# Kernel optimization log

Measured on AMD Instinct MI355X. Metric: run time of the kernel, lower is better.

Reference implementation:

```python
import jax, jax.numpy as jnp
import numpy as np

B, S, D = 4, 2048, 1024
H, DK = 16, 64
NUM_BUCKETS = 32
MAX_DISTANCE = 128
EPS = 1e-6


def _relative_position_bucket(q_len, kv_len):
    # causal (bidirectional=False) T5 bucketization
    ctx = jnp.arange(q_len, dtype=jnp.int32)[:, None]
    mem = jnp.arange(kv_len, dtype=jnp.int32)[None, :]
    rp = mem - ctx                       # [q, kv]
    rp = -jnp.minimum(rp, 0)             # nonnegative distances to the past
    max_exact = NUM_BUCKETS // 2
    is_small = rp < max_exact
    rp_safe = jnp.maximum(rp, 1).astype(jnp.float32)
    large = max_exact + (
        jnp.log(rp_safe / max_exact) / np.log(MAX_DISTANCE / max_exact) * (NUM_BUCKETS - max_exact)
    ).astype(jnp.int32)
    large = jnp.minimum(large, NUM_BUCKETS - 1)
    return jnp.where(is_small, rp, large)  # [q, kv] int32 in [0, NUM_BUCKETS)


def setup_inputs() -> dict:
    key = jax.random.key(0)
    k1, k2, k3, k4 = jax.random.split(key, 4)
    hidden_states = jax.random.normal(k1, (B, S, D), dtype=jnp.float32)
    sequence_mask = jnp.ones((B, S), dtype=bool)
    rms_w = jnp.ones((D,), dtype=jnp.float32)
    W_qkv = jax.random.normal(k2, (D, 3 * H * DK), dtype=jnp.float32) * (D ** -0.5)
    W_o = jax.random.normal(k3, (H * DK, D), dtype=jnp.float32) * ((H * DK) ** -0.5)
    rel_bias = jax.random.normal(k4, (NUM_BUCKETS, H), dtype=jnp.float32)
    return {"hidden_states": hidden_states, "sequence_mask": sequence_mask,
            "rms_w": rms_w, "W_qkv": W_qkv, "W_o": W_o, "rel_bias": rel_bias}


def reference(hidden_states, sequence_mask, rms_w, W_qkv, W_o, rel_bias):
    # RMSNorm
    var = jnp.mean(hidden_states * hidden_states, axis=-1, keepdims=True)
    normed = hidden_states * jax.lax.rsqrt(var + EPS) * rms_w

    # QKV projection -> [B, S, 3, H, DK] -> [B, H, S, DK] each
    qkv = (normed @ W_qkv).reshape(B, S, 3, H, DK)
    q = jnp.transpose(qkv[:, :, 0], (0, 2, 1, 3))
    k = jnp.transpose(qkv[:, :, 1], (0, 2, 1, 3))
    v = jnp.transpose(qkv[:, :, 2], (0, 2, 1, 3))

    # relative position bias: gather [S,S,H] -> [1,H,S,S]
    bucket = _relative_position_bucket(S, S)
    pos_bias = jnp.transpose(rel_bias[bucket], (2, 0, 1))[None]

    # scores (note: T5 does NOT scale by 1/sqrt(dk))
    scores = jnp.einsum("bhqd,bhkd->bhqk", q, k) + pos_bias

    # causal mask combined with sequence mask (True = attend)
    causal = jnp.tril(jnp.ones((S, S), dtype=bool))
    mask = causal[None, None] & sequence_mask[:, None, None, :]
    scores = jnp.where(mask, scores, jnp.finfo(scores.dtype).min)

    attn = jax.nn.softmax(scores.astype(jnp.float32), axis=-1).astype(scores.dtype)
    # dropout p=0 / eval mode -> identity
    ctx = jnp.einsum("bhqk,bhkd->bhqd", attn, v)          # [B,H,S,DK]
    ctx = jnp.transpose(ctx, (0, 2, 1, 3)).reshape(B, S, H * DK)
    out = hidden_states + ctx @ W_o                        # residual
    return out
```

## Files before the change

kernel.cpp:

```cpp
#include <hip/hip_runtime.h>
#include <math.h>


typedef unsigned short ushort_t;
typedef __attribute__((ext_vector_type(8))) short bfrag;
typedef __attribute__((ext_vector_type(4))) float ffrag;

#define MFMA16(a, b, c) __builtin_amdgcn_mfma_f32_16x16x32_bf16((a), (b), (c), 0, 0, 0)
#define LOG2E 1.4426950408889634f

__device__ __forceinline__ void load_lds16(const ushort_t* g, ushort_t* l) {
  __builtin_amdgcn_global_load_lds(
      (const __attribute__((address_space(1))) unsigned int*)g,
      (__attribute__((address_space(3))) unsigned int*)l, 16, 0, 0);
}

__device__ __forceinline__ ushort_t f2bf(float f) {
  union { float f; unsigned u; } x; x.f = f;
  unsigned r = x.u + 0x7FFFu + ((x.u >> 16) & 1u);
  return (ushort_t)(r >> 16);
}
__device__ __forceinline__ float bf2f(ushort_t u) {
  union { unsigned u; float f; } x; x.u = ((unsigned)u) << 16; return x.f;
}
__device__ __forceinline__ unsigned cvtpk(float lo, float hi) {
  unsigned r;
  asm("v_cvt_pk_bf16_f32 %0, %1, %2" : "=v"(r) : "v"(lo), "v"(hi));
  return r;
}
__device__ __forceinline__ float exp2fast(float x) {
  return __builtin_amdgcn_exp2f(x);
}

__global__ __launch_bounds__(256) void norm_cvt_kernel(
    const float* __restrict__ hidden, const float* __restrict__ rms_w,
    ushort_t* __restrict__ normed) {
  const int w = threadIdx.x >> 6, lane = threadIdx.x & 63;
  const int row = blockIdx.x * 4 + w;
  const float* p = hidden + (size_t)row * 1024;
  float4 v[4];
  float s = 0.f;
#pragma unroll
  for (int i = 0; i < 4; ++i) {
    v[i] = *(const float4*)(p + (lane + i * 64) * 4);
    s += v[i].x * v[i].x + v[i].y * v[i].y + v[i].z * v[i].z + v[i].w * v[i].w;
  }
#pragma unroll
  for (int off = 1; off < 64; off <<= 1) s += __shfl_xor(s, off, 64);
  const float scale = rsqrtf(s * (1.0f / 1024.0f) + 1e-6f);
#pragma unroll
  for (int i = 0; i < 4; ++i) {
    const int c0 = (lane + i * 64) * 4;
    float4 wv = *(const float4*)(rms_w + c0);
    ushort4 u;
    u.x = f2bf(v[i].x * scale * wv.x);
    u.y = f2bf(v[i].y * scale * wv.y);
    u.z = f2bf(v[i].z * scale * wv.z);
    u.w = f2bf(v[i].w * scale * wv.w);
    *(ushort4*)(normed + (size_t)row * 1024 + c0) = u;
  }
}

__global__ __launch_bounds__(256) void transpose_cvt_kernel(
    const float* __restrict__ in, ushort_t* __restrict__ out, int R, int C) {
  __shared__ float tile[32][33];
  const int r0 = blockIdx.y * 32, c0 = blockIdx.x * 32;
  const int tr = threadIdx.x >> 5, tc = threadIdx.x & 31;
#pragma unroll
  for (int i = 0; i < 32; i += 8)
    tile[tr + i][tc] = in[(size_t)(r0 + tr + i) * C + c0 + tc];
  __syncthreads();
#pragma unroll
  for (int i = 0; i < 32; i += 8)
    out[(size_t)(c0 + tr + i) * R + r0 + tc] = f2bf(tile[tc][tr + i]);
}

__global__ __launch_bounds__(256) void qkv_mfma_kernel(
    const ushort_t* __restrict__ A, const ushort_t* __restrict__ Bt,
    ushort_t* __restrict__ qbf, ushort_t* __restrict__ kbf,
    ushort_t* __restrict__ vtbf) {
  __shared__ ushort_t At[128 * 32];
  __shared__ ushort_t Bs[128 * 32];
  const int tid = threadIdx.x, w = tid >> 6, lane = tid & 63;
  const int quad = lane >> 4, ln = lane & 15;
  const int wr = w >> 1, wc = w & 1;
  const int m0 = blockIdx.y * 128, n0 = blockIdx.x * 128;
  const int srow = lane >> 2, scol = (lane & 3) * 8;

  ffrag acc[4][4];
#pragma unroll
  for (int i = 0; i < 4; ++i)
#pragma unroll
    for (int j = 0; j < 4; ++j) acc[i][j] = (ffrag)0.f;

  for (int kb = 0; kb < 1024; kb += 32) {
#pragma unroll
    for (int p = 0; p < 2; ++p) {
      load_lds16(A + (size_t)(m0 + (w * 2 + p) * 16 + srow) * 1024 + kb + scol,
                 At + (w * 2 + p) * 512);
      load_lds16(Bt + (size_t)(n0 + (w * 2 + p) * 16 + srow) * 1024 + kb + scol,
                 Bs + (w * 2 + p) * 512);
    }
    __syncthreads();
    bfrag a[4], b[4];
#pragma unroll
    for (int mi = 0; mi < 4; ++mi)
      a[mi] = *(const bfrag*)(At + (wr * 64 + mi * 16 + ln) * 32 + quad * 8);
#pragma unroll
    for (int ni = 0; ni < 4; ++ni)
      b[ni] = *(const bfrag*)(Bs + (wc * 64 + ni * 16 + ln) * 32 + quad * 8);
#pragma unroll
    for (int mi = 0; mi < 4; ++mi)
#pragma unroll
      for (int ni = 0; ni < 4; ++ni)
        acc[mi][ni] = MFMA16(a[mi], b[ni], acc[mi][ni]);
    __syncthreads();
  }

  const int b_idx = m0 >> 11;
  const int cbase = n0 + wc * 64 + ln;
#pragma unroll
  for (int mi = 0; mi < 4; ++mi) {
    const int sbase = (m0 & 2047) + wr * 64 + mi * 16 + quad * 4;
#pragma unroll
    for (int ni = 0; ni < 4; ++ni) {
      const int c = cbase + ni * 16;
      const int three = c >> 10, rem = c & 1023;
      const int h = rem >> 6, dk = rem & 63;
      if (three == 2) {
        ushort4 u;
        u.x = f2bf(acc[mi][ni][0]); u.y = f2bf(acc[mi][ni][1]);
        u.z = f2bf(acc[mi][ni][2]); u.w = f2bf(acc[mi][ni][3]);
        *(ushort4*)(vtbf + ((size_t)(b_idx * 16 + h) * 64 + dk) * 2048 + sbase) = u;
      } else {
        const float sc = (three == 0) ? 1.0f : LOG2E;
        ushort_t* dst = (three == 0 ? qbf : kbf) +
                        ((size_t)(b_idx * 16 + h) * 2048 + sbase) * 64 + dk;
        dst[0]   = f2bf(acc[mi][ni][0] * sc);
        dst[64]  = f2bf(acc[mi][ni][1] * sc);
        dst[128] = f2bf(acc[mi][ni][2] * sc);
        dst[192] = f2bf(acc[mi][ni][3] * sc);
      }
    }
  }
}

__global__ __launch_bounds__(256) void attn_mfma_kernel(
    const ushort_t* __restrict__ qbf, const ushort_t* __restrict__ kbf,
    const ushort_t* __restrict__ vtbf, const float* __restrict__ rel_bias,
    ushort_t* __restrict__ ctx) {
  __shared__ ushort_t Kt[2][2][64][32];
  __shared__ ushort_t Vt[2][64][32];
  __shared__ ushort_t Pt[64][64];
  __shared__ ushort_t bias_t[2048];

  const int tid = threadIdx.x, w = tid >> 6, lane = tid & 63;
  const int quad = lane >> 4, ln = lane & 15;
  const int id = blockIdx.x;
  const int bh = id & 63;
  const int pr = id >> 6;
  const int h = bh & 15;

  for (int dist = tid; dist < 2048; dist += 256) {
    int bucket;
    if (dist < 16) bucket = dist;
    else {
      bucket = 16 + (int)(logf((float)dist * (1.0f / 16.0f)) * (16.0f / logf(8.0f)));
      if (bucket > 31) bucket = 31;
    }
    bias_t[dist] = f2bf(rel_bias[bucket * 16 + h] * LOG2E);
  }
  const float c31 = bf2f(f2bf(rel_bias[31 * 16 + h] * LOG2E));

  const size_t khead = (size_t)bh * 2048 * 64;
  const int sidx = lane >> 2;
  const int scol8 = ((lane & 3) ^ ((lane >> 3) & 3)) * 8;
  const int rsw = ((ln >> 1) & 3) * 8;
  const int psw = (ln & 7) * 8;

  for (int ph = 0; ph < 2; ++ph) {
    const int qb = ph ? (31 - pr) : pr;
    const int q0w = qb * 64 + w * 16;

    bfrag aq[2];
#pragma unroll
    for (int kf = 0; kf < 2; ++kf)
      aq[kf] = *(const bfrag*)(qbf + ((size_t)bh * 2048 + q0w + ln) * 64 +
                               kf * 32 + quad * 8);

    ffrag o[4];
#pragma unroll
    for (int nd = 0; nd < 4; ++nd) o[nd] = (ffrag)0.f;
    float m_run = -3.0e38f, l_run = 0.f;

#pragma unroll
    for (int p2 = 0; p2 < 2; ++p2) {
      const int idx = p2 * 4 + w, panel = idx >> 2, rb = idx & 3;
      load_lds16(kbf + khead + (size_t)(rb * 16 + sidx) * 64 + panel * 32 + scol8,
                 &Kt[0][0][0][0] + idx * 512);
    }
    __syncthreads();

    int cur = 0;
    for (int j = 0; j <= qb; ++j) {
      const int key0 = j * 64;

#pragma unroll
      for (int p2 = 0; p2 < 2; ++p2) {
        const int idx = p2 * 4 + w, panel = idx >> 2, rb = idx & 3;
        load_lds16(vtbf + khead + (size_t)(rb * 16 + sidx) * 2048 + key0 + panel * 32 + scol8,
                   &Vt[0][0][0] + idx * 512);
      }
      if (j < qb) {
        const int nk0 = key0 + 64;
#pragma unroll
        for (int p2 = 0; p2 < 2; ++p2) {
          const int idx = p2 * 4 + w, panel = idx >> 2, rb = idx & 3;
          load_lds16(kbf + khead + (size_t)(nk0 + rb * 16 + sidx) * 64 + panel * 32 + scol8,
                     &Kt[cur ^ 1][0][0][0] + idx * 512);
        }
      }

      ffrag s[4];
#pragma unroll
      for (int mi = 0; mi < 4; ++mi) s[mi] = (ffrag)0.f;
      __builtin_amdgcn_s_setprio(1);
#pragma unroll
      for (int kf = 0; kf < 2; ++kf)
#pragma unroll
        for (int mi = 0; mi < 4; ++mi) {
          bfrag ak = *(const bfrag*)&Kt[cur][kf][mi * 16 + ln][(quad * 8) ^ rsw];
          s[mi] = MFMA16(ak, aq[kf], s[mi]);
        }
      __builtin_amdgcn_s_setprio(0);

      const bool fastT = (key0 + 176 <= q0w);
      float mxe;
      if (fastT) {
        float mx = s[0][0];
#pragma unroll
        for (int mi = 0; mi < 4; ++mi)
#pragma unroll
          for (int r = 0; r < 4; ++r) mx = fmaxf(mx, s[mi][r]);
        mx = fmaxf(mx, __shfl_xor(mx, 16, 64));
        mx = fmaxf(mx, __shfl_xor(mx, 32, 64));
        mxe = mx + c31;
      } else {
        const int q = q0w + ln;
        float mx = -3.0e38f;
#pragma unroll
        for (int mi = 0; mi < 4; ++mi) {
          const int keyb = key0 + mi * 16 + quad * 4;
#pragma unroll
          for (int r = 0; r < 4; ++r) {
            const int dist = q - (keyb + r);
            const int db = dist < 0 ? 0 : dist;
            const float val = (dist < 0) ? -3.0e38f : (s[mi][r] + bf2f(bias_t[db]));
            s[mi][r] = val;
            mx = fmaxf(mx, val);
          }
        }
        mx = fmaxf(mx, __shfl_xor(mx, 16, 64));
        mx = fmaxf(mx, __shfl_xor(mx, 32, 64));
        mxe = mx;
      }

      const float sbias = fastT ? c31 : 0.f;
      const int grow = !__all(mxe <= m_run + 8.0f);
      float alpha = 1.0f, mnew = m_run;
      if (grow) {
        mnew = fmaxf(m_run, mxe);
        alpha = exp2fast(m_run - mnew);
      }
      const float sh = mnew - sbias;
      float ps = 0.f;
#pragma unroll
      for (int mi = 0; mi < 4; ++mi)
#pragma unroll
        for (int r = 0; r < 4; ++r) {
          const float pv = exp2fast(s[mi][r] - sh);
          s[mi][r] = pv;
          ps += pv;
        }
      ps += __shfl_xor(ps, 16, 64);
      ps += __shfl_xor(ps, 32, 64);
      if (grow) {
        l_run = l_run * alpha + ps;
        m_run = mnew;
#pragma unroll
        for (int r = 0; r < 4; ++r) {
          const float af = __shfl(alpha, quad * 4 + r, 64);
#pragma unroll
          for (int nd = 0; nd < 4; ++nd) o[nd][r] *= af;
        }
      } else {
        l_run += ps;
      }

      {
        ushort_t* prow = &Pt[w * 16 + ln][0];
#pragma unroll
        for (int mi = 0; mi < 4; ++mi) {
          uint2 pk;
          pk.x = cvtpk(s[mi][0], s[mi][1]);
          pk.y = cvtpk(s[mi][2], s[mi][3]);
          *(uint2*)(prow + ((mi * 16 + quad * 4) ^ psw)) = pk;
        }
      }

      if (j < qb) {
        asm volatile("s_waitcnt vmcnt(2)" ::: "memory");
      } else {
        asm volatile("s_waitcnt vmcnt(0)" ::: "memory");
      }
      __builtin_amdgcn_s_barrier();

      __builtin_amdgcn_s_setprio(1);
#pragma unroll
      for (int kf = 0; kf < 2; ++kf) {
        bfrag ap = *(const bfrag*)&Pt[w * 16 + ln][(kf * 32 + quad * 8) ^ psw];
#pragma unroll
        for (int nd = 0; nd < 4; ++nd) {
          bfrag bv = *(const bfrag*)&Vt[kf][nd * 16 + ln][(quad * 8) ^ rsw];
          o[nd] = MFMA16(ap, bv, o[nd]);
        }
      }
      __builtin_amdgcn_s_setprio(0);

      __syncthreads();
      cur ^= 1;
    }

    ffrag inv;
#pragma unroll
    for (int r = 0; r < 4; ++r)
      inv[r] = 1.0f / __shfl(l_run, quad * 4 + r, 64);
    const int s0 = q0w + quad * 4;
#pragma unroll
    for (int nd = 0; nd < 4; ++nd)
#pragma unroll
      for (int r = 0; r < 4; ++r)
        ctx[((size_t)(bh >> 4) * 2048 + s0 + r) * 1024 + h * 64 + nd * 16 + ln] =
            f2bf(o[nd][r] * inv[r]);
  }
}

__global__ __launch_bounds__(256) void out_mfma_kernel(
    const ushort_t* __restrict__ A, const ushort_t* __restrict__ Bt,
    const float* __restrict__ hidden, float* __restrict__ out) {
  __shared__ ushort_t At[128 * 32];
  __shared__ ushort_t Bs[128 * 32];
  const int tid = threadIdx.x, w = tid >> 6, lane = tid & 63;
  const int quad = lane >> 4, ln = lane & 15;
  const int wr = w >> 1, wc = w & 1;
  const int m0 = blockIdx.y * 128, n0 = blockIdx.x * 128;
  const int srow = lane >> 2, scol = (lane & 3) * 8;

  ffrag acc[4][4];
#pragma unroll
  for (int i = 0; i < 4; ++i)
#pragma unroll
    for (int j = 0; j < 4; ++j) acc[i][j] = (ffrag)0.f;

  for (int kb = 0; kb < 1024; kb += 32) {
#pragma unroll
    for (int p = 0; p < 2; ++p) {
      load_lds16(A + (size_t)(m0 + (w * 2 + p) * 16 + srow) * 1024 + kb + scol,
                 At + (w * 2 + p) * 512);
      load_lds16(Bt + (size_t)(n0 + (w * 2 + p) * 16 + srow) * 1024 + kb + scol,
                 Bs + (w * 2 + p) * 512);
    }
    __syncthreads();
    bfrag a[4], b[4];
#pragma unroll
    for (int mi = 0; mi < 4; ++mi)
      a[mi] = *(const bfrag*)(At + (wr * 64 + mi * 16 + ln) * 32 + quad * 8);
#pragma unroll
    for (int ni = 0; ni < 4; ++ni)
      b[ni] = *(const bfrag*)(Bs + (wc * 64 + ni * 16 + ln) * 32 + quad * 8);
#pragma unroll
    for (int mi = 0; mi < 4; ++mi)
#pragma unroll
      for (int ni = 0; ni < 4; ++ni)
        acc[mi][ni] = MFMA16(a[mi], b[ni], acc[mi][ni]);
    __syncthreads();
  }
#pragma unroll
  for (int mi = 0; mi < 4; ++mi) {
    const int m = m0 + wr * 64 + mi * 16 + quad * 4;
#pragma unroll
    for (int ni = 0; ni < 4; ++ni) {
      const int c = n0 + wc * 64 + ni * 16 + ln;
#pragma unroll
      for (int r = 0; r < 4; ++r) {
        const size_t off = (size_t)(m + r) * 1024 + c;
        out[off] = acc[mi][ni][r] + hidden[off];
      }
    }
  }
}

extern "C" void kernel_launch(void* const* d_in, const int* in_sizes, int n_in,
                              void* d_out, int out_size, void* d_ws, size_t ws_size,
                              hipStream_t stream) {
  const size_t NORMED = (size_t)8192 * 1024;
  const size_t WQKVT  = (size_t)3072 * 1024;
  const size_t WOT    = (size_t)1024 * 1024;
  const size_t QKVE   = (size_t)64 * 2048 * 64;
  const size_t need = (NORMED + WQKVT + WOT + 3 * QKVE + NORMED) * 2;
  if (ws_size < need) return;

  const float* hidden   = (const float*)d_in[0];
  const float* rms_w    = (const float*)d_in[2];
  const float* Wqkv     = (const float*)d_in[3];
  const float* Wo       = (const float*)d_in[4];
  const float* rel_bias = (const float*)d_in[5];
  float* out = (float*)d_out;

  ushort_t* normed = (ushort_t*)d_ws;
  ushort_t* wqkvt  = normed + NORMED;
  ushort_t* wot    = wqkvt + WQKVT;
  ushort_t* qbf    = wot + WOT;
  ushort_t* kbf    = qbf + QKVE;
  ushort_t* vtbf   = kbf + QKVE;
  ushort_t* ctx    = vtbf + QKVE;

  norm_cvt_kernel<<<2048, 256, 0, stream>>>(hidden, rms_w, normed);
  transpose_cvt_kernel<<<dim3(96, 32), 256, 0, stream>>>(Wqkv, wqkvt, 1024, 3072);
  transpose_cvt_kernel<<<dim3(32, 32), 256, 0, stream>>>(Wo, wot, 1024, 1024);
  qkv_mfma_kernel<<<dim3(24, 64), 256, 0, stream>>>(normed, wqkvt, qbf, kbf, vtbf);
  attn_mfma_kernel<<<1024, 256, 0, stream>>>(qbf, kbf, vtbf, rel_bias, ctx);
  out_mfma_kernel<<<dim3(8, 64), 256, 0, stream>>>(ctx, wot, hidden, out);
}
```

Before: 301.8 us.

## Restructure attention to 128-query blocks of 8 waves and XCD-swizzle GEMM grids

The attention kernel now runs 512-thread blocks, each covering 128 query rows of one head. K/V tiles are shared across 8 waves and double-buffered with one barrier per iteration, replacing the paired-phase 64-row scheme. The row sum is computed with an MFMA against a ones vector instead of shuffles, and there is a third bias path for tiles in the middle distance range. The QKV and output GEMMs remap 1D block ids so each XCD gets a contiguous band of rows, for L2 locality. Risks: load imbalance because blocks are ordered from largest to smallest qb without the pairing, and waves on the upper rows skip compute but still wait at barriers.

```diff
diff --git a/kernel.cpp b/kernel.cpp
--- a/kernel.cpp
+++ b/kernel.cpp
@@ -84,7 +84,10 @@
   const int tid = threadIdx.x, w = tid >> 6, lane = tid & 63;
   const int quad = lane >> 4, ln = lane & 15;
   const int wr = w >> 1, wc = w & 1;
-  const int m0 = blockIdx.y * 128, n0 = blockIdx.x * 128;
+  const int id = blockIdx.x;
+  const int xcd = id & 7, t = id >> 3;
+  const int by = xcd * 8 + t / 24, bx = t % 24;
+  const int m0 = by * 128, n0 = bx * 128;
   const int srow = lane >> 2, scol = (lane & 3) * 8;
 
   ffrag acc[4][4];
@@ -145,23 +148,25 @@
   }
 }
 
-__global__ __launch_bounds__(256) void attn_mfma_kernel(
+__global__ __launch_bounds__(512, 6) void attn_mfma_kernel(
     const ushort_t* __restrict__ qbf, const ushort_t* __restrict__ kbf,
     const ushort_t* __restrict__ vtbf, const float* __restrict__ rel_bias,
     ushort_t* __restrict__ ctx) {
   __shared__ ushort_t Kt[2][2][64][32];
-  __shared__ ushort_t Vt[2][64][32];
-  __shared__ ushort_t Pt[64][64];
+  __shared__ ushort_t Vt[2][2][64][32];
+  __shared__ ushort_t Pt[128][64];
   __shared__ ushort_t bias_t[2048];
 
   const int tid = threadIdx.x, w = tid >> 6, lane = tid & 63;
   const int quad = lane >> 4, ln = lane & 15;
   const int id = blockIdx.x;
   const int bh = id & 63;
-  const int pr = id >> 6;
+  const int qb = 15 - (id >> 6);
   const int h = bh & 15;
-
-  for (int dist = tid; dist < 2048; dist += 256) {
+  const int nt = 2 * qb + 2;
+  const int q0w = qb * 128 + w * 16;
+
+  for (int dist = tid; dist < 2048; dist += 512) {
     int bucket;
     if (dist < 16) bucket = dist;
     else {
@@ -171,56 +176,51 @@
     bias_t[dist] = f2bf(rel_bias[bucket * 16 + h] * LOG2E);
   }
   const float c31 = bf2f(f2bf(rel_bias[31 * 16 + h] * LOG2E));
+  __syncthreads();
 
   const size_t khead = (size_t)bh * 2048 * 64;
-  const int sidx = lane >> 2;
-  const int scol8 = ((lane & 3) ^ ((lane >> 3) & 3)) * 8;
+  const int skf = tid >> 8;
+  const int srow = (tid >> 2) & 63;
+  const int ssw = ((tid & 3) ^ ((srow >> 1) & 3)) * 8;
   const int rsw = ((ln >> 1) & 3) * 8;
   const int psw = (ln & 7) * 8;
 
-  for (int ph = 0; ph < 2; ++ph) {
-    const int qb = ph ? (31 - pr) : pr;
-    const int q0w = qb * 64 + w * 16;
-
-    bfrag aq[2];
-#pragma unroll
-    for (int kf = 0; kf < 2; ++kf)
-      aq[kf] = *(const bfrag*)(qbf + ((size_t)bh * 2048 + q0w + ln) * 64 +
-                               kf * 32 + quad * 8);
-
-    ffrag o[4];
-#pragma unroll
-    for (int nd = 0; nd < 4; ++nd) o[nd] = (ffrag)0.f;
-    float m_run = -3.0e38f, l_run = 0.f;
-
-#pragma unroll
-    for (int p2 = 0; p2 < 2; ++p2) {
-      const int idx = p2 * 4 + w, panel = idx >> 2, rb = idx & 3;
-      load_lds16(kbf + khead + (size_t)(rb * 16 + sidx) * 64 + panel * 32 + scol8,
-                 &Kt[0][0][0][0] + idx * 512);
-    }
-    __syncthreads();
-
-    int cur = 0;
-    for (int j = 0; j <= qb; ++j) {
-      const int key0 = j * 64;
-
-#pragma unroll
-      for (int p2 = 0; p2 < 2; ++p2) {
-        const int idx = p2 * 4 + w, panel = idx >> 2, rb = idx & 3;
-        load_lds16(vtbf + khead + (size_t)(rb * 16 + sidx) * 2048 + key0 + panel * 32 + scol8,
-                   &Vt[0][0][0] + idx * 512);
-      }
-      if (j < qb) {
-        const int nk0 = key0 + 64;
-#pragma unroll
-        for (int p2 = 0; p2 < 2; ++p2) {
-          const int idx = p2 * 4 + w, panel = idx >> 2, rb = idx & 3;
-          load_lds16(kbf + khead + (size_t)(nk0 + rb * 16 + sidx) * 64 + panel * 32 + scol8,
-                     &Kt[cur ^ 1][0][0][0] + idx * 512);
-        }
-      }
-
+  bfrag aq[2];
+#pragma unroll
+  for (int kf = 0; kf < 2; ++kf)
+    aq[kf] = *(const bfrag*)(qbf + ((size_t)bh * 2048 + q0w + ln) * 64 +
+                             kf * 32 + quad * 8);
+
+  bfrag ones;
+#pragma unroll
+  for (int i = 0; i < 8; ++i) ones[i] = (short)0x3F80;
+
+  ffrag o[4], l_acc;
+#pragma unroll
+  for (int nd = 0; nd < 4; ++nd) o[nd] = (ffrag)0.f;
+  l_acc = (ffrag)0.f;
+  float m_run = -3.0e38f;
+
+  load_lds16(kbf + khead + (size_t)srow * 64 + skf * 32 + ssw,
+             &Kt[0][0][0][0] + tid * 8);
+  load_lds16(vtbf + khead + (size_t)srow * 2048 + 0 + skf * 32 + ssw,
+             &Vt[0][0][0][0] + tid * 8);
+
+  int cur = 0;
+  for (int j = 0; j < nt; ++j) {
+    const int key0 = j * 64;
+    asm volatile("s_waitcnt vmcnt(0)" ::: "memory");
+    __builtin_amdgcn_s_barrier();
+
+    if (j + 1 < nt) {
+      const int nk0 = key0 + 64;
+      load_lds16(kbf + khead + (size_t)(nk0 + srow) * 64 + skf * 32 + ssw,
+                 &Kt[cur ^ 1][0][0][0] + tid * 8);
+      load_lds16(vtbf + khead + (size_t)srow * 2048 + nk0 + skf * 32 + ssw,
+                 &Vt[cur ^ 1][0][0][0] + tid * 8);
+    }
+
+    if (key0 <= q0w + 15) {
       ffrag s[4];
 #pragma unroll
       for (int mi = 0; mi < 4; ++mi) s[mi] = (ffrag)0.f;
@@ -234,20 +234,13 @@
         }
       __builtin_amdgcn_s_setprio(0);
 
+      const bool diagT = (key0 + 63 > q0w);
       const bool fastT = (key0 + 176 <= q0w);
-      float mxe;
+      float sbias = 0.f;
       if (fastT) {
-        float mx = s[0][0];
-#pragma unroll
-        for (int mi = 0; mi < 4; ++mi)
-#pragma unroll
-          for (int r = 0; r < 4; ++r) mx = fmaxf(mx, s[mi][r]);
-        mx = fmaxf(mx, __shfl_xor(mx, 16, 64));
-        mx = fmaxf(mx, __shfl_xor(mx, 32, 64));
-        mxe = mx + c31;
-      } else {
+        sbias = c31;
+      } else if (diagT) {
         const int q = q0w + ln;
-        float mx = -3.0e38f;
 #pragma unroll
         for (int mi = 0; mi < 4; ++mi) {
           const int keyb = key0 + mi * 16 + quad * 4;
@@ -255,47 +248,47 @@
           for (int r = 0; r < 4; ++r) {
             const int dist = q - (keyb + r);
             const int db = dist < 0 ? 0 : dist;
-            const float val = (dist < 0) ? -3.0e38f : (s[mi][r] + bf2f(bias_t[db]));
-            s[mi][r] = val;
-            mx = fmaxf(mx, val);
+            s[mi][r] = (dist < 0) ? -3.0e38f : (s[mi][r] + bf2f(bias_t[db]));
           }
         }
-        mx = fmaxf(mx, __shfl_xor(mx, 16, 64));
-        mx = fmaxf(mx, __shfl_xor(mx, 32, 64));
-        mxe = mx;
-      }
-
-      const float sbias = fastT ? c31 : 0.f;
-      const int grow = !__all(mxe <= m_run + 8.0f);
-      float alpha = 1.0f, mnew = m_run;
-      if (grow) {
-        mnew = fmaxf(m_run, mxe);
-        alpha = exp2fast(m_run - mnew);
-      }
-      const float sh = mnew - sbias;
-      float ps = 0.f;
-#pragma unroll
-      for (int mi = 0; mi < 4; ++mi)
-#pragma unroll
-        for (int r = 0; r < 4; ++r) {
-          const float pv = exp2fast(s[mi][r] - sh);
-          s[mi][r] = pv;
-          ps += pv;
-        }
-      ps += __shfl_xor(ps, 16, 64);
-      ps += __shfl_xor(ps, 32, 64);
-      if (grow) {
-        l_run = l_run * alpha + ps;
+      } else {
+        const int q = q0w + ln;
+#pragma unroll
+        for (int mi = 0; mi < 4; ++mi) {
+          const int keyb = key0 + mi * 16 + quad * 4;
+#pragma unroll
+          for (int r = 0; r < 4; ++r)
+            s[mi][r] += bf2f(bias_t[q - (keyb + r)]);
+        }
+      }
+
+      float m0_ = fmaxf(fmaxf(s[0][0], s[0][1]), fmaxf(s[0][2], s[0][3]));
+      float m1_ = fmaxf(fmaxf(s[1][0], s[1][1]), fmaxf(s[1][2], s[1][3]));
+      float m2_ = fmaxf(fmaxf(s[2][0], s[2][1]), fmaxf(s[2][2], s[2][3]));
+      float m3_ = fmaxf(fmaxf(s[3][0], s[3][1]), fmaxf(s[3][2], s[3][3]));
+      float mx = fmaxf(fmaxf(m0_, m1_), fmaxf(m2_, m3_));
+      mx = fmaxf(mx, __shfl_xor(mx, 16, 64));
+      mx = fmaxf(mx, __shfl_xor(mx, 32, 64));
+      const float mxe = mx + sbias;
+
+      if (!__all(mxe <= m_run + 8.0f)) {
+        const float mnew = fmaxf(m_run, mxe);
+        const float alpha = exp2fast(m_run - mnew);
         m_run = mnew;
 #pragma unroll
         for (int r = 0; r < 4; ++r) {
           const float af = __shfl(alpha, quad * 4 + r, 64);
 #pragma unroll
           for (int nd = 0; nd < 4; ++nd) o[nd][r] *= af;
-        }
-      } else {
-        l_run += ps;
-      }
+          l_acc[r] *= af;
+        }
+      }
+      const float sh = m_run - sbias;
+#pragma unroll
+      for (int mi = 0; mi < 4; ++mi)
+#pragma unroll
+        for (int r = 0; r < 4; ++r)
+          s[mi][r] = exp2fast(s[mi][r] - sh);
 
       {
         ushort_t* prow = &Pt[w * 16 + ln][0];
@@ -308,41 +301,32 @@
         }
       }
 
-      if (j < qb) {
-        asm volatile("s_waitcnt vmcnt(2)" ::: "memory");
-      } else {
-        asm volatile("s_waitcnt vmcnt(0)" ::: "memory");
-      }
-      __builtin_amdgcn_s_barrier();
-
       __builtin_amdgcn_s_setprio(1);
 #pragma unroll
       for (int kf = 0; kf < 2; ++kf) {
         bfrag ap = *(const bfrag*)&Pt[w * 16 + ln][(kf * 32 + quad * 8) ^ psw];
+        l_acc = MFMA16(ap, ones, l_acc);
 #pragma unroll
         for (int nd = 0; nd < 4; ++nd) {
-          bfrag bv = *(const bfrag*)&Vt[kf][nd * 16 + ln][(quad * 8) ^ rsw];
+          bfrag bv = *(const bfrag*)&Vt[cur][kf][nd * 16 + ln][(quad * 8) ^ rsw];
           o[nd] = MFMA16(ap, bv, o[nd]);
         }
       }
       __builtin_amdgcn_s_setprio(0);
-
-      __syncthreads();
-      cur ^= 1;
-    }
-
-    ffrag inv;
+    }
+    cur ^= 1;
+  }
+
+  ffrag inv;
+#pragma unroll
+  for (int r = 0; r < 4; ++r) inv[r] = 1.0f / l_acc[r];
+  const int s0 = q0w + quad * 4;
+#pragma unroll
+  for (int nd = 0; nd < 4; ++nd)
 #pragma unroll
     for (int r = 0; r < 4; ++r)
-      inv[r] = 1.0f / __shfl(l_run, quad * 4 + r, 64);
-    const int s0 = q0w + quad * 4;
-#pragma unroll
-    for (int nd = 0; nd < 4; ++nd)
-#pragma unroll
-      for (int r = 0; r < 4; ++r)
-        ctx[((size_t)(bh >> 4) * 2048 + s0 + r) * 1024 + h * 64 + nd * 16 + ln] =
-            f2bf(o[nd][r] * inv[r]);
-  }
+      ctx[((size_t)(bh >> 4) * 2048 + s0 + r) * 1024 + h * 64 + nd * 16 + ln] =
+          f2bf(o[nd][r] * inv[r]);
 }
 
 __global__ __launch_bounds__(256) void out_mfma_kernel(
@@ -353,7 +337,10 @@
   const int tid = threadIdx.x, w = tid >> 6, lane = tid & 63;
   const int quad = lane >> 4, ln = lane & 15;
   const int wr = w >> 1, wc = w & 1;
-  const int m0 = blockIdx.y * 128, n0 = blockIdx.x * 128;
+  const int id = blockIdx.x;
+  const int xcd = id & 7, t = id >> 3;
+  const int by = xcd * 8 + (t >> 3), bx = t & 7;
+  const int m0 = by * 128, n0 = bx * 128;
   const int srow = lane >> 2, scol = (lane & 3) * 8;
 
   ffrag acc[4][4];
@@ -428,7 +415,7 @@
   norm_cvt_kernel<<<2048, 256, 0, stream>>>(hidden, rms_w, normed);
   transpose_cvt_kernel<<<dim3(96, 32), 256, 0, stream>>>(Wqkv, wqkvt, 1024, 3072);
   transpose_cvt_kernel<<<dim3(32, 32), 256, 0, stream>>>(Wo, wot, 1024, 1024);
-  qkv_mfma_kernel<<<dim3(24, 64), 256, 0, stream>>>(normed, wqkvt, qbf, kbf, vtbf);
-  attn_mfma_kernel<<<1024, 256, 0, stream>>>(qbf, kbf, vtbf, rel_bias, ctx);
-  out_mfma_kernel<<<dim3(8, 64), 256, 0, stream>>>(ctx, wot, hidden, out);
-}
+  qkv_mfma_kernel<<<1536, 256, 0, stream>>>(normed, wqkvt, qbf, kbf, vtbf);
+  attn_mfma_kernel<<<1024, 512, 0, stream>>>(qbf, kbf, vtbf, rel_bias, ctx);
+  out_mfma_kernel<<<512, 256, 0, stream>>>(ctx, wot, hidden, out);
+}
```

After: 278.5 us. 1.08x faster.
